# Kernel tuning notes

Hardware: AMD Instinct MI355X
Metric: run time of the kernel (lower is better)

The kernel has to match this reference:

```python
import jax, jax.numpy as jnp
import numpy as np

# Dims: L layers, batch B, seq S, model dim D, heads H, ffn FF
L, B, S, D, H = 8, 2, 1024, 1024, 16
FF = 4 * D
HD = D // H
EPS = 1e-5  # torch LayerNorm default


def setup_inputs() -> dict:
    key = jax.random.key(0)
    ks = jax.random.split(key, 6)
    g = lambda k, shape, s: jax.random.normal(k, shape, jnp.float32) * s
    return {
        "x": g(ks[0], (B, S, D), 1.0),
        # True = masked out (code passes ~attn_mask to F.sdpa): causal mask
        "attn_mask": jnp.triu(jnp.ones((S, S), bool), 1),
        "qkv_w": g(ks[1], (L, 3 * D, D), 0.02),
        "qkv_b": jnp.zeros((L, 3 * D), jnp.float32),
        "out_w": g(ks[2], (L, D, D), 0.02),
        "out_b": jnp.zeros((L, D), jnp.float32),
        "w1": g(ks[3], (L, FF, D), 0.02),
        "b1": jnp.zeros((L, FF), jnp.float32),
        "w2": g(ks[4], (L, D, FF), 0.02),
        "b2": jnp.zeros((L, D), jnp.float32),
        "ln1_w": jnp.ones((L, D), jnp.float32),
        "ln1_b": jnp.zeros((L, D), jnp.float32),
        "ln2_w": jnp.ones((L, D), jnp.float32),
        "ln2_b": jnp.zeros((L, D), jnp.float32),
    }


def _layer_norm(x, w, b):
    m = jnp.mean(x, axis=-1, keepdims=True)
    v = jnp.var(x, axis=-1, keepdims=True)
    return (x - m) * jax.lax.rsqrt(v + EPS) * w + b


def _block(x, mask, qw, qb, ow, ob, w1, b1, w2, b2, l1w, l1b, l2w, l2b):
    # fused QKV projection: [B,S,3D]
    qkv = jnp.einsum("bsd,ed->bse", x, qw) + qb
    q, k, v = jnp.split(qkv, 3, axis=-1)
    k_cache, v_cache = k, v  # caches are stored pre-head-split [B,S,D]
    to_heads = lambda t: t.reshape(B, S, H, HD).transpose(0, 2, 1, 3)
    qh, kh, vh = to_heads(q), to_heads(k), to_heads(v)
    scores = jnp.einsum("bhqd,bhkd->bhqk", qh, kh) / jnp.sqrt(jnp.float32(HD))
    scores = jnp.where(mask, -jnp.inf, scores)  # mask True = disallowed
    attn = jnp.einsum("bhqk,bhkd->bhqd", jax.nn.softmax(scores, axis=-1), vh)
    attn = attn.transpose(0, 2, 1, 3).reshape(B, S, D)
    attn = jnp.einsum("bsd,ed->bse", attn, ow) + ob
    # post-LN residual + ReLU MLP + post-LN (padding_mask=None branch)
    x = _layer_norm(x + attn, l1w, l1b)
    h = jnp.einsum("bsf,df->bsd", jax.nn.relu(jnp.einsum("bsd,fd->bsf", x, w1) + b1), w2) + b2
    x = _layer_norm(x + h, l2w, l2b)
    return x, k_cache, v_cache


def reference(x, attn_mask, qkv_w, qkv_b, out_w, out_b, w1, b1, w2, b2,
              ln1_w, ln1_b, ln2_w, ln2_b):
    def step(carry, p):
        xc = carry
        xo, kc, vc = _block(xc, attn_mask, *p)
        return xo, (kc, vc)

    params = (qkv_w, qkv_b, out_w, out_b, w1, b1, w2, b2,
              ln1_w, ln1_b, ln2_w, ln2_b)
    x_out, (k_cache, v_cache) = jax.lax.scan(step, x, params)
    return x_out, k_cache, v_cache
```

## Files before the change

### kernel.cpp

```cpp
#include <hip/hip_runtime.h>
#include <cstdint>
#include <cstddef>
#include <math.h>

#define LL  8
#define BB  2
#define SS  1024
#define DD  1024
#define HH  16
#define HD  64
#define FFD 4096
#define BSD (BB*SS*DD)

typedef __attribute__((ext_vector_type(4))) float f32x4;
typedef __attribute__((ext_vector_type(8))) short bf16x8;
typedef __attribute__((ext_vector_type(4))) short bf16x4;

__device__ __forceinline__ unsigned short f2bf(float f) {
    unsigned u = __float_as_uint(f);
    unsigned r = (u + 0x7fffu + ((u >> 16) & 1u)) >> 16;
    return (unsigned short)r;
}
__device__ __forceinline__ float bf2f(unsigned short u) {
    return __uint_as_float((unsigned)u << 16);
}

#define GLD16(gsrc, ldst) \
    __builtin_amdgcn_global_load_lds((const __attribute__((address_space(1))) void*)(gsrc), \
                                     (__attribute__((address_space(3))) void*)(ldst), 16, 0, 0)

__device__ __forceinline__ void xcd_swizzle(int& bx, int& by)
{
    const int nx  = gridDim.x;
    const int nwg = nx * gridDim.y;
    const int flat = by * nx + bx;
    const int cpx = nwg >> 3;
    const int swz = (flat & 7) * cpx + (flat >> 3);
    bx = swz % nx;
    by = swz / nx;
}

__global__ __launch_bounds__(256)
void cvt_bf16(const float* __restrict__ in, unsigned short* __restrict__ out)
{
    size_t i = (size_t)blockIdx.x * 256 + threadIdx.x;
    float4 v = *(const float4*)(in + i * 4);
    ushort4 o;
    o.x = f2bf(v.x); o.y = f2bf(v.y); o.z = f2bf(v.z); o.w = f2bf(v.w);
    *(ushort4*)(out + i * 4) = o;
}

__global__ __launch_bounds__(256)
void cvt_x(const float* __restrict__ in, float* __restrict__ outf,
           unsigned short* __restrict__ outb)
{
    size_t i = (size_t)blockIdx.x * 256 + threadIdx.x;
    float4 v = *(const float4*)(in + i * 4);
    *(float4*)(outf + i * 4) = v;
    ushort4 o;
    o.x = f2bf(v.x); o.y = f2bf(v.y); o.z = f2bf(v.z); o.w = f2bf(v.w);
    *(ushort4*)(outb + i * 4) = o;
}

__global__ __launch_bounds__(512)
void gemm_bf16(const unsigned short* __restrict__ A, const unsigned short* __restrict__ W,
               const float* __restrict__ bias,
               float* __restrict__ C, unsigned short* __restrict__ Cb,
               float* __restrict__ Ck, float* __restrict__ Cv,
               unsigned short* __restrict__ Kb16, unsigned short* __restrict__ Vb16,
               int M, int N, int klen, int mode)
{
    __shared__ unsigned short lds[2][2 * 128 * 64];

    int bx = blockIdx.x, by = blockIdx.y;
    xcd_swizzle(bx, by);

    const int tid  = threadIdx.x;
    const int m0   = by * 128;
    const int n0   = bx * 128;
    const int kbase= blockIdx.z * klen;
    const int lane = tid & 63;
    const int w    = tid >> 6;
    const int wr   = w >> 2;
    const int wc   = w & 3;
    const int lr   = lane & 15;
    const int kq   = lane >> 4;

    const int K = (mode == 3) ? (klen * gridDim.z) : klen;
    const int T = klen >> 6;

    const int srow0 = tid >> 3;
    const int spc0  = tid & 7;
    const int slc0  = spc0 ^ (srow0 & 7);
    const int srow1 = (tid + 512) >> 3;
    const int spc1  = (tid + 512) & 7;
    const int slc1  = spc1 ^ (srow1 & 7);

    #define STAGE_TILE(ti, dst)                                                   \
        do {                                                                      \
            const int kc = kbase + (ti) * 64;                                     \
            GLD16(A + (size_t)(m0 + srow0) * K + kc + slc0 * 8, (dst) + tid * 8); \
            GLD16(A + (size_t)(m0 + srow1) * K + kc + slc1 * 8, (dst) + 4096 + tid * 8); \
            GLD16(W + (size_t)(n0 + srow0) * K + kc + slc0 * 8, (dst) + 8192 + tid * 8); \
            GLD16(W + (size_t)(n0 + srow1) * K + kc + slc1 * 8, (dst) + 12288 + tid * 8); \
        } while (0)

    f32x4 acc[4][2];
    #pragma unroll
    for (int i = 0; i < 4; ++i)
        #pragma unroll
        for (int j = 0; j < 2; ++j) {
            f32x4 z = {0.f, 0.f, 0.f, 0.f};
            acc[i][j] = z;
        }

    STAGE_TILE(0, lds[0]);
    STAGE_TILE(1, lds[1]);

    for (int t = 0; t < T; ++t) {
        unsigned short* cb = lds[t & 1];

        if (t == T - 1) {
            asm volatile("s_waitcnt vmcnt(0)\n\ts_barrier" ::: "memory");
        } else {
            asm volatile("s_waitcnt vmcnt(4)\n\ts_barrier" ::: "memory");
        }

        bf16x8 a[4], b[2], a2[4], b2[2];
        #pragma unroll
        for (int mf = 0; mf < 4; ++mf) {
            const int r = wr * 64 + mf * 16 + lr;
            const int pc = kq ^ (r & 7);
            a[mf] = *(const bf16x8*)(cb + r * 64 + pc * 8);
        }
        #pragma unroll
        for (int nf = 0; nf < 2; ++nf) {
            const int r = wc * 32 + nf * 16 + lr;
            const int pc = kq ^ (r & 7);
            b[nf] = *(const bf16x8*)(cb + 8192 + r * 64 + pc * 8);
        }
        #pragma unroll
        for (int mf = 0; mf < 4; ++mf) {
            const int r = wr * 64 + mf * 16 + lr;
            const int pc = (4 + kq) ^ (r & 7);
            a2[mf] = *(const bf16x8*)(cb + r * 64 + pc * 8);
        }
        #pragma unroll
        for (int nf = 0; nf < 2; ++nf) {
            const int r = wc * 32 + nf * 16 + lr;
            const int pc = (4 + kq) ^ (r & 7);
            b2[nf] = *(const bf16x8*)(cb + 8192 + r * 64 + pc * 8);
        }

        __builtin_amdgcn_s_setprio(1);
        #pragma unroll
        for (int mf = 0; mf < 4; ++mf)
            #pragma unroll
            for (int nf = 0; nf < 2; ++nf)
                acc[mf][nf] = __builtin_amdgcn_mfma_f32_16x16x32_bf16(
                    a[mf], b[nf], acc[mf][nf], 0, 0, 0);
        #pragma unroll
        for (int mf = 0; mf < 4; ++mf)
            #pragma unroll
            for (int nf = 0; nf < 2; ++nf)
                acc[mf][nf] = __builtin_amdgcn_mfma_f32_16x16x32_bf16(
                    a2[mf], b2[nf], acc[mf][nf], 0, 0, 0);
        __builtin_amdgcn_s_setprio(0);

        asm volatile("s_waitcnt lgkmcnt(0)\n\ts_barrier" ::: "memory");
        if (t + 2 < T) STAGE_TILE(t + 2, cb);
    }
    #undef STAGE_TILE

    const int seg = n0 >> 10;
    #pragma unroll
    for (int nf = 0; nf < 2; ++nf) {
        const int cl = wc * 32 + nf * 16 + lr;
        const float bv = (mode == 3) ? 0.f : bias[n0 + cl];
        #pragma unroll
        for (int mf = 0; mf < 4; ++mf) {
            #pragma unroll
            for (int r = 0; r < 4; ++r) {
                const int row = m0 + wr * 64 + mf * 16 + kq * 4 + r;
                const float val = acc[mf][nf][r] + bv;
                if (mode == 2) {
                    const int col = (n0 & 1023) + cl;
                    float* dstf = (seg == 1) ? Ck : ((seg == 2) ? Cv : nullptr);
                    unsigned short* dstb = (seg == 0) ? Cb : ((seg == 1) ? Kb16 : Vb16);
                    if (dstf) dstf[(size_t)row * DD + col] = val;
                    dstb[(size_t)row * DD + col] = f2bf(val);
                } else if (mode == 1) {
                    Cb[(size_t)row * N + n0 + cl] = f2bf(fmaxf(val, 0.f));
                } else {
                    Cb[(size_t)blockIdx.z * M * N + (size_t)row * N + n0 + cl] = f2bf(val);
                }
            }
        }
    }
}

__global__ __launch_bounds__(512)
void attn_mfma(const unsigned short* __restrict__ Qb, const unsigned short* __restrict__ Kb,
               const unsigned short* __restrict__ Vb, unsigned short* __restrict__ ctxb)
{
    int bx = blockIdx.x, by = blockIdx.y;
    xcd_swizzle(bx, by);
    const int qt = bx;
    const int h  = by;
    const int b  = blockIdx.z;
    const int tid  = threadIdx.x;
    const int lane = tid & 63;
    const int w    = tid >> 6;
    const int lr   = lane & 15;
    const int hi   = lane >> 4;

    __shared__ unsigned short smem[128 * 68 + 64 * 136 + 8 * 16 * 136];
    unsigned short* Ks = smem;
    unsigned short* Vt = smem + 128 * 68;
    unsigned short* Pl = smem + 128 * 68 + 64 * 136 + w * 16 * 136;

    const int qg0 = qt * 128 + w * 16;

    bf16x8 qa[2];
    {
        const unsigned short* qp = Qb + ((size_t)(b * SS + qg0 + lr)) * DD + h * HD;
        qa[0] = *(const bf16x8*)(qp + hi * 8);
        qa[1] = *(const bf16x8*)(qp + 32 + hi * 8);
    }

    f32x4 accO[4];
    #pragma unroll
    for (int t = 0; t < 4; ++t) { f32x4 z = {0.f,0.f,0.f,0.f}; accO[t] = z; }
    float m_run[4], l_run[4];
    #pragma unroll
    for (int r = 0; r < 4; ++r) { m_run[r] = -INFINITY; l_run[r] = 0.f; }

    const int nch = qt + 1;
    for (int c = 0; c < nch; ++c) {
        __syncthreads();
        const unsigned short* kb = Kb + ((size_t)(b * SS + c * 128)) * DD + h * HD;
        const unsigned short* vb = Vb + ((size_t)(b * SS + c * 128)) * DD + h * HD;
        #pragma unroll
        for (int i = 0; i < 2; ++i) {
            int e = tid + i * 512;
            int r  = e >> 3, ch = e & 7;
            bf16x8 kv = *(const bf16x8*)(kb + (size_t)r * DD + ch * 8);
            *(bf16x4*)(Ks + r * 68 + ch * 8)     = __builtin_shufflevector(kv, kv, 0,1,2,3);
            *(bf16x4*)(Ks + r * 68 + ch * 8 + 4) = __builtin_shufflevector(kv, kv, 4,5,6,7);
            int k  = e & 127, d0 = (e >> 7) * 8;
            bf16x8 vv = *(const bf16x8*)(vb + (size_t)k * DD + d0);
            #pragma unroll
            for (int j = 0; j < 8; ++j)
                Vt[(d0 + j) * 136 + k] = (unsigned short)vv[j];
        }
        __syncthreads();

        f32x4 sa[8];
        #pragma unroll
        for (int t = 0; t < 8; ++t) { f32x4 z = {0.f,0.f,0.f,0.f}; sa[t] = z; }
        #pragma unroll
        for (int t = 0; t < 8; ++t) {
            #pragma unroll
            for (int s = 0; s < 2; ++s) {
                const unsigned short* bp = Ks + (t * 16 + lr) * 68 + s * 32 + hi * 8;
                bf16x4 b0 = *(const bf16x4*)bp;
                bf16x4 b1 = *(const bf16x4*)(bp + 4);
                bf16x8 bb = __builtin_shufflevector(b0, b1, 0,1,2,3,4,5,6,7);
                sa[t] = __builtin_amdgcn_mfma_f32_16x16x32_bf16(qa[s], bb, sa[t], 0, 0, 0);
            }
        }
        if (c == qt) {
            #pragma unroll
            for (int t = 0; t < 8; ++t) {
                #pragma unroll
                for (int r = 0; r < 4; ++r) {
                    const int kg = c * 128 + t * 16 + lr;
                    const int qg = qg0 + hi * 4 + r;
                    sa[t][r] = (kg > qg) ? -1e30f : sa[t][r] * 0.125f;
                }
            }
        } else {
            #pragma unroll
            for (int t = 0; t < 8; ++t)
                #pragma unroll
                for (int r = 0; r < 4; ++r)
                    sa[t][r] *= 0.125f;
        }
        #pragma unroll
        for (int r = 0; r < 4; ++r) {
            float mx = -INFINITY;
            #pragma unroll
            for (int t = 0; t < 8; ++t) mx = fmaxf(mx, sa[t][r]);
            mx = fmaxf(mx, __shfl_xor(mx, 1));
            mx = fmaxf(mx, __shfl_xor(mx, 2));
            mx = fmaxf(mx, __shfl_xor(mx, 4));
            mx = fmaxf(mx, __shfl_xor(mx, 8));
            const float mn = fmaxf(m_run[r], mx);
            float sum = 0.f;
            #pragma unroll
            for (int t = 0; t < 8; ++t) {
                float p = __expf(sa[t][r] - mn);
                sa[t][r] = p;
                sum += p;
            }
            sum += __shfl_xor(sum, 1);
            sum += __shfl_xor(sum, 2);
            sum += __shfl_xor(sum, 4);
            sum += __shfl_xor(sum, 8);
            const float sc = __expf(m_run[r] - mn);
            l_run[r] = l_run[r] * sc + sum;
            m_run[r] = mn;
            #pragma unroll
            for (int t = 0; t < 4; ++t) accO[t][r] *= sc;
        }
        #pragma unroll
        for (int t = 0; t < 8; ++t)
            #pragma unroll
            for (int r = 0; r < 4; ++r)
                Pl[(hi * 4 + r) * 136 + t * 16 + lr] = f2bf(sa[t][r]);

        #pragma unroll
        for (int s = 0; s < 4; ++s) {
            const unsigned short* ap = Pl + lr * 136 + s * 32 + hi * 8;
            bf16x4 a0 = *(const bf16x4*)ap;
            bf16x4 a1 = *(const bf16x4*)(ap + 4);
            bf16x8 aa = __builtin_shufflevector(a0, a1, 0,1,2,3,4,5,6,7);
            #pragma unroll
            for (int t = 0; t < 4; ++t) {
                const unsigned short* bp = Vt + (t * 16 + lr) * 136 + s * 32 + hi * 8;
                bf16x4 b0 = *(const bf16x4*)bp;
                bf16x4 b1 = *(const bf16x4*)(bp + 4);
                bf16x8 bb = __builtin_shufflevector(b0, b1, 0,1,2,3,4,5,6,7);
                accO[t] = __builtin_amdgcn_mfma_f32_16x16x32_bf16(aa, bb, accO[t], 0, 0, 0);
            }
        }
    }

    float inv[4];
    #pragma unroll
    for (int r = 0; r < 4; ++r) inv[r] = 1.f / l_run[r];

    __syncthreads();
    float* Of = (float*)smem;
    #pragma unroll
    for (int t = 0; t < 4; ++t)
        #pragma unroll
        for (int r = 0; r < 4; ++r)
            Of[(w * 16 + hi * 4 + r) * 68 + t * 16 + lr] = accO[t][r] * inv[r];
    __syncthreads();
    #pragma unroll
    for (int i = 0; i < 2; ++i) {
        int e = tid + i * 512;
        int r = e >> 3, ch = e & 7;
        const float* src = Of + r * 68 + ch * 8;
        float4 v0 = *(const float4*)(src);
        float4 v1 = *(const float4*)(src + 4);
        bf16x8 o;
        o[0] = (short)f2bf(v0.x); o[1] = (short)f2bf(v0.y);
        o[2] = (short)f2bf(v0.z); o[3] = (short)f2bf(v0.w);
        o[4] = (short)f2bf(v1.x); o[5] = (short)f2bf(v1.y);
        o[6] = (short)f2bf(v1.z); o[7] = (short)f2bf(v1.w);
        *(bf16x8*)(ctxb + ((size_t)(b * SS + qt * 128 + r)) * DD + h * HD + ch * 8) = o;
    }
}

__global__ __launch_bounds__(256)
void ln_kernel(const float* __restrict__ x, float* __restrict__ xo,
               const unsigned short* __restrict__ P,
               const float* __restrict__ bias,
               const float* __restrict__ w, const float* __restrict__ b,
               unsigned short* __restrict__ xb)
{
    const size_t PS = (size_t)BSD;
    const int row = blockIdx.x;
    const int t   = threadIdx.x;
    const int d0  = t * 4;
    const float* xr = x + (size_t)row * DD;
    float* xor_ = xo + (size_t)row * DD;
    unsigned short* xbr = xb + (size_t)row * DD;
    const size_t base = (size_t)row * DD + d0;

    float4 xv = *(const float4*)(xr + d0);
    float4 bv = *(const float4*)(bias + d0);
    float z[4] = {xv.x + bv.x, xv.y + bv.y, xv.z + bv.z, xv.w + bv.w};
    #pragma unroll
    for (int p = 0; p < 4; ++p) {
        ushort4 pv = *(const ushort4*)(P + base + p * PS);
        z[0] += bf2f(pv.x); z[1] += bf2f(pv.y); z[2] += bf2f(pv.z); z[3] += bf2f(pv.w);
    }
    float s = z[0] + z[1] + z[2] + z[3];
    float ss = z[0]*z[0] + z[1]*z[1] + z[2]*z[2] + z[3]*z[3];

    #pragma unroll
    for (int off = 32; off; off >>= 1) {
        s  += __shfl_down(s, off);
        ss += __shfl_down(ss, off);
    }
    __shared__ float sbuf[4], ssbuf[4];
    const int wave = t >> 6, lane = t & 63;
    if (lane == 0) { sbuf[wave] = s; ssbuf[wave] = ss; }
    __syncthreads();
    if (t == 0) {
        float S = 0.f, SSum = 0.f;
        #pragma unroll
        for (int i = 0; i < 4; ++i) { S += sbuf[i]; SSum += ssbuf[i]; }
        float mean = S * (1.f / 1024.f);
        float var  = SSum * (1.f / 1024.f) - mean * mean;
        sbuf[0]  = mean;
        ssbuf[0] = rsqrtf(var + 1e-5f);
    }
    __syncthreads();
    const float mean = sbuf[0], rstd = ssbuf[0];

    float4 wv = *(const float4*)(w + d0);
    float4 bb = *(const float4*)(b + d0);
    float o0 = (z[0] - mean) * rstd * wv.x + bb.x;
    float o1 = (z[1] - mean) * rstd * wv.y + bb.y;
    float o2 = (z[2] - mean) * rstd * wv.z + bb.z;
    float o3 = (z[3] - mean) * rstd * wv.w + bb.w;
    *(float4*)(xor_ + d0) = make_float4(o0, o1, o2, o3);
    ushort4 ob4;
    ob4.x = f2bf(o0); ob4.y = f2bf(o1); ob4.z = f2bf(o2); ob4.w = f2bf(o3);
    *(ushort4*)(xbr + d0) = ob4;
}

extern "C" void kernel_launch(void* const* d_in, const int* in_sizes, int n_in,
                              void* d_out, int out_size, void* d_ws, size_t ws_size,
                              hipStream_t stream)
{
    const float* x_in  = (const float*)d_in[0];
    const float* qkv_w = (const float*)d_in[2];
    const float* qkv_b = (const float*)d_in[3];
    const float* out_w = (const float*)d_in[4];
    const float* out_b = (const float*)d_in[5];
    const float* w1    = (const float*)d_in[6];
    const float* b1    = (const float*)d_in[7];
    const float* w2    = (const float*)d_in[8];
    const float* b2    = (const float*)d_in[9];
    const float* ln1w  = (const float*)d_in[10];
    const float* ln1b  = (const float*)d_in[11];
    const float* ln2w  = (const float*)d_in[12];
    const float* ln2b  = (const float*)d_in[13];

    float* out_x = (float*)d_out;
    float* out_k = out_x + (size_t)BSD;
    float* out_v = out_k + (size_t)LL * BSD;

    const size_t MEG = 1024 * 1024;
    float* ws = (float*)d_ws;
    float*          xbuf  = ws;
    unsigned short* part16= (unsigned short*)(ws + 2 * MEG);
    unsigned short* xb16  = (unsigned short*)(ws + 6 * MEG);
    unsigned short* ctxb  = (unsigned short*)(ws + 7 * MEG);
    unsigned short* hb16  = (unsigned short*)(ws + 8 * MEG);
    unsigned short* qb16  = hb16;
    unsigned short* kb16  = hb16 + 2 * MEG;
    unsigned short* vb16  = hb16 + 4 * MEG;
    unsigned short* wAll  = (unsigned short*)(ws + 12 * MEG);

    unsigned short* qkvW = wAll;
    unsigned short* outW = wAll + 24 * MEG;
    unsigned short* w1W  = wAll + 32 * MEG;
    unsigned short* w2W  = wAll + 64 * MEG;

    cvt_bf16<<<24 * MEG / 1024, 256, 0, stream>>>(qkv_w, qkvW);
    cvt_bf16<<< 8 * MEG / 1024, 256, 0, stream>>>(out_w, outW);
    cvt_bf16<<<32 * MEG / 1024, 256, 0, stream>>>(w1,    w1W);
    cvt_bf16<<<32 * MEG / 1024, 256, 0, stream>>>(w2,    w2W);
    cvt_x<<<BSD / 1024, 256, 0, stream>>>(x_in, xbuf, xb16);

    const int M = BB * SS;

    for (int l = 0; l < LL; ++l) {
        const float* qb  = qkv_b + (size_t)l * 3 * DD;
        const float* ob  = out_b + (size_t)l * DD;
        const float* b1l = b1    + (size_t)l * FFD;
        const float* b2l = b2    + (size_t)l * DD;
        const unsigned short* qwl = qkvW + (size_t)l * 3 * DD * DD;
        const unsigned short* owl = outW + (size_t)l * DD * DD;
        const unsigned short* w1l = w1W  + (size_t)l * FFD * DD;
        const unsigned short* w2l = w2W  + (size_t)l * DD * FFD;
        float* kc = out_k + (size_t)l * BSD;
        float* vc = out_v + (size_t)l * BSD;

        gemm_bf16<<<dim3(3 * DD / 128, M / 128, 1), 512, 0, stream>>>(
            xb16, qwl, qb, nullptr, qb16, kc, vc, kb16, vb16, M, 3 * DD, DD, 2);

        attn_mfma<<<dim3(SS / 128, HH, BB), 512, 0, stream>>>(qb16, kb16, vb16, ctxb);

        gemm_bf16<<<dim3(DD / 128, M / 128, 4), 512, 0, stream>>>(
            ctxb, owl, nullptr, nullptr, part16, nullptr, nullptr, nullptr, nullptr,
            M, DD, DD / 4, 3);

        ln_kernel<<<M, 256, 0, stream>>>(xbuf, xbuf, part16, ob,
                                         ln1w + (size_t)l * DD, ln1b + (size_t)l * DD, xb16);

        gemm_bf16<<<dim3(FFD / 128, M / 128, 1), 512, 0, stream>>>(
            xb16, w1l, b1l, nullptr, hb16, nullptr, nullptr, nullptr, nullptr,
            M, FFD, DD, 1);

        gemm_bf16<<<dim3(DD / 128, M / 128, 4), 512, 0, stream>>>(
            hb16, w2l, nullptr, nullptr, part16, nullptr, nullptr, nullptr, nullptr,
            M, DD, FFD / 4, 3);

        float* xo = (l == LL - 1) ? out_x : xbuf;
        ln_kernel<<<M, 256, 0, stream>>>(xbuf, xo, part16, b2l,
                                         ln2w + (size_t)l * DD, ln2b + (size_t)l * DD, xb16);
    }
}
```

Before: 1.243 ms.

## Merge weight conversions, skip fp32 x copy, read K directly from global

```diff
diff --git a/kernel.cpp b/kernel.cpp
--- a/kernel.cpp
+++ b/kernel.cpp
@@ -51,15 +51,23 @@
 }
 
 __global__ __launch_bounds__(256)
-void cvt_x(const float* __restrict__ in, float* __restrict__ outf,
-           unsigned short* __restrict__ outb)
-{
+void cvt_weights(const float* __restrict__ qkv, const float* __restrict__ ow,
+                 const float* __restrict__ w1, const float* __restrict__ w2,
+                 unsigned short* __restrict__ out)
+{
+    const size_t MEGc = 1024 * 1024;
     size_t i = (size_t)blockIdx.x * 256 + threadIdx.x;
-    float4 v = *(const float4*)(in + i * 4);
-    *(float4*)(outf + i * 4) = v;
+    size_t e = i * 4;
+    const float* src;
+    size_t off;
+    if (e < 24 * MEGc)      { src = qkv; off = 0; }
+    else if (e < 32 * MEGc) { src = ow;  off = 24 * MEGc; }
+    else if (e < 64 * MEGc) { src = w1;  off = 32 * MEGc; }
+    else                    { src = w2;  off = 64 * MEGc; }
+    float4 v = *(const float4*)(src + (e - off));
     ushort4 o;
     o.x = f2bf(v.x); o.y = f2bf(v.y); o.z = f2bf(v.z); o.w = f2bf(v.w);
-    *(ushort4*)(outb + i * 4) = o;
+    *(ushort4*)(out + e) = o;
 }
 
 __global__ __launch_bounds__(512)
@@ -214,10 +222,9 @@
     const int lr   = lane & 15;
     const int hi   = lane >> 4;
 
-    __shared__ unsigned short smem[128 * 68 + 64 * 136 + 8 * 16 * 136];
-    unsigned short* Ks = smem;
-    unsigned short* Vt = smem + 128 * 68;
-    unsigned short* Pl = smem + 128 * 68 + 64 * 136 + w * 16 * 136;
+    __shared__ unsigned short smem[64 * 136 + 8 * 16 * 136];
+    unsigned short* Vt = smem;
+    unsigned short* Pl = smem + 64 * 136 + w * 16 * 136;
 
     const int qg0 = qt * 128 + w * 16;
 
@@ -243,10 +250,6 @@
         #pragma unroll
         for (int i = 0; i < 2; ++i) {
             int e = tid + i * 512;
-            int r  = e >> 3, ch = e & 7;
-            bf16x8 kv = *(const bf16x8*)(kb + (size_t)r * DD + ch * 8);
-            *(bf16x4*)(Ks + r * 68 + ch * 8)     = __builtin_shufflevector(kv, kv, 0,1,2,3);
-            *(bf16x4*)(Ks + r * 68 + ch * 8 + 4) = __builtin_shufflevector(kv, kv, 4,5,6,7);
             int k  = e & 127, d0 = (e >> 7) * 8;
             bf16x8 vv = *(const bf16x8*)(vb + (size_t)k * DD + d0);
             #pragma unroll
@@ -262,10 +265,7 @@
         for (int t = 0; t < 8; ++t) {
             #pragma unroll
             for (int s = 0; s < 2; ++s) {
-                const unsigned short* bp = Ks + (t * 16 + lr) * 68 + s * 32 + hi * 8;
-                bf16x4 b0 = *(const bf16x4*)bp;
-                bf16x4 b1 = *(const bf16x4*)(bp + 4);
-                bf16x8 bb = __builtin_shufflevector(b0, b1, 0,1,2,3,4,5,6,7);
+                bf16x8 bb = *(const bf16x8*)(kb + (size_t)(t * 16 + lr) * DD + s * 32 + hi * 8);
                 sa[t] = __builtin_amdgcn_mfma_f32_16x16x32_bf16(qa[s], bb, sa[t], 0, 0, 0);
             }
         }
@@ -463,11 +463,8 @@
     unsigned short* w1W  = wAll + 32 * MEG;
     unsigned short* w2W  = wAll + 64 * MEG;
 
-    cvt_bf16<<<24 * MEG / 1024, 256, 0, stream>>>(qkv_w, qkvW);
-    cvt_bf16<<< 8 * MEG / 1024, 256, 0, stream>>>(out_w, outW);
-    cvt_bf16<<<32 * MEG / 1024, 256, 0, stream>>>(w1,    w1W);
-    cvt_bf16<<<32 * MEG / 1024, 256, 0, stream>>>(w2,    w2W);
-    cvt_x<<<BSD / 1024, 256, 0, stream>>>(x_in, xbuf, xb16);
+    cvt_weights<<<96 * MEG / 1024, 256, 0, stream>>>(qkv_w, out_w, w1, w2, wAll);
+    cvt_bf16<<<BSD / 1024, 256, 0, stream>>>(x_in, xb16);
 
     const int M = BB * SS;
 
@@ -492,7 +489,8 @@
             ctxb, owl, nullptr, nullptr, part16, nullptr, nullptr, nullptr, nullptr,
             M, DD, DD / 4, 3);
 
-        ln_kernel<<<M, 256, 0, stream>>>(xbuf, xbuf, part16, ob,
+        const float* xin_l = (l == 0) ? x_in : xbuf;
+        ln_kernel<<<M, 256, 0, stream>>>(xin_l, xbuf, part16, ob,
                                          ln1w + (size_t)l * DD, ln1b + (size_t)l * DD, xb16);
 
         gemm_bf16<<<dim3(FFD / 128, M / 128, 1), 512, 0, stream>>>(
```

New measurement: 1.375 ms. +10.6%, slower.
